# Performance work log

Hardware: AMD Instinct MI355X
Metric: run time of the kernel (lower is better)

Reference implementation:

```python
import jax, jax.numpy as jnp
import numpy as np

N_NODES = 100000
N_EDGES = 1600000
F_IN = 128
H = 128
L = 3
BN_EPS = 1e-5
NORM_EPS = 1e-12


def setup_inputs() -> dict:
    key = jax.random.key(0)
    ks = jax.random.split(key, 32)
    def rn(k, shape, s=0.05):
        return jax.random.normal(k, shape, dtype=jnp.float32) * s
    inp = {
        'x': jax.random.normal(ks[0], (N_NODES, F_IN), dtype=jnp.float32),
        'edge_index': jax.random.randint(ks[1], (2, N_EDGES), 0, N_NODES, dtype=jnp.int32),
        # node encoder
        'enc_w': rn(ks[2], (H, F_IN)), 'enc_b': rn(ks[3], (H,)),
        # per-layer SAGEConv params (stacked over layers)
        'lin_l_w': rn(ks[4], (L, H, H)), 'lin_l_b': rn(ks[5], (L, H)),
        'lin_r_w': rn(ks[6], (L, H, H)),
        # batch norms (eval mode: running stats)
        'bn_gamma': jnp.ones((L, H), jnp.float32), 'bn_beta': jnp.zeros((L, H), jnp.float32),
        'bn_mean': jnp.zeros((L, H), jnp.float32), 'bn_var': jnp.ones((L, H), jnp.float32),
        # output head
        'out_w1': rn(ks[7], (H, H)), 'out_b1': rn(ks[8], (H,)),
        'out_w2': rn(ks[9], (1, H)), 'out_b2': rn(ks[10], (1,)),
        # cost head
        'cost_w1': rn(ks[11], (H // 2, H)), 'cost_b1': rn(ks[12], (H // 2,)),
        'cost_w2': rn(ks[13], (1, H // 2)), 'cost_b2': rn(ks[14], (1,)),
        # bullwhip head
        'bw_w1': rn(ks[15], (H // 2, H)), 'bw_b1': rn(ks[16], (H // 2,)),
        'bw_w2': rn(ks[17], (1, H // 2)), 'bw_b2': rn(ks[18], (1,)),
    }
    return inp


def _sage_conv(h, src, dst, wl, bl, wr):
    # PyG SAGEConv (aggr='mean', normalize=True): lin_l(mean_j x_j) + lin_r(x_i), then L2 normalize
    msg_sum = jax.ops.segment_sum(h[src], dst, num_segments=N_NODES)  # [N, H]
    deg = jax.ops.segment_sum(jnp.ones((src.shape[0],), h.dtype), dst, num_segments=N_NODES)
    mean = msg_sum / jnp.maximum(deg, 1.0)[:, None]
    out = mean @ wl.T + bl + h @ wr.T
    norm = jnp.linalg.norm(out, axis=-1, keepdims=True)
    return out / jnp.maximum(norm, NORM_EPS)


def reference(x, edge_index, enc_w, enc_b, lin_l_w, lin_l_b, lin_r_w,
              bn_gamma, bn_beta, bn_mean, bn_var,
              out_w1, out_b1, out_w2, out_b2,
              cost_w1, cost_b1, cost_w2, cost_b2,
              bw_w1, bw_b1, bw_w2, bw_b2):
    src, dst = edge_index[0], edge_index[1]
    h = jax.nn.relu(x @ enc_w.T + enc_b)  # dropout is identity in eval
    for i in range(L):
        h = _sage_conv(h, src, dst, lin_l_w[i], lin_l_b[i], lin_r_w[i])
        # BatchNorm1d in eval mode
        h = (h - bn_mean[i]) * (bn_gamma[i] / jnp.sqrt(bn_var[i] + BN_EPS)) + bn_beta[i]
        h = jax.nn.relu(h)
    order = jax.nn.relu(h @ out_w1.T + out_b1) @ out_w2.T + out_b2
    cost = jax.nn.relu(h @ cost_w1.T + cost_b1) @ cost_w2.T + cost_b2
    bullwhip = jax.nn.relu(h @ bw_w1.T + bw_b1) @ bw_w2.T + bw_b2
    return (order, cost, bullwhip, h)
```

## Files before the change

### kernel.cpp

```cpp
#include <hip/hip_runtime.h>

#define NN 100000
#define NE 1600000
#define TN 16
#define NBK 391
#define BCAP 5120
#define CTILE 8192

static constexpr float BN_EPS = 1e-5f;
static constexpr float NORM_EPS = 1e-12f;

typedef unsigned int u32;
typedef unsigned short u16;
typedef __attribute__((ext_vector_type(8))) short short8;
typedef __attribute__((ext_vector_type(4))) float f32x4;

__device__ __forceinline__ float bflo(u32 u) {
    u32 v = u << 16; float f; __builtin_memcpy(&f, &v, 4); return f;
}
__device__ __forceinline__ float bfhi(u32 u) {
    u32 v = u & 0xffff0000u; float f; __builtin_memcpy(&f, &v, 4); return f;
}
__device__ __forceinline__ u32 packbf(float a, float b) {
    u32 ua, ub; __builtin_memcpy(&ua, &a, 4); __builtin_memcpy(&ub, &b, 4);
    u32 ra = (ua + 0x7fffu + ((ua >> 16) & 1u)) >> 16;
    u32 rb = (ub + 0x7fffu + ((ub >> 16) & 1u)) & 0xffff0000u;
    return ra | rb;
}
__device__ __forceinline__ u16 f2bf(float a) {
    u32 ua; __builtin_memcpy(&ua, &a, 4);
    return (u16)((ua + 0x7fffu + ((ua >> 16) & 1u)) >> 16);
}
__device__ __forceinline__ void acc8(float* s, uint4 v) {
    s[0] += bflo(v.x); s[1] += bfhi(v.x);
    s[2] += bflo(v.y); s[3] += bfhi(v.y);
    s[4] += bflo(v.z); s[5] += bfhi(v.z);
    s[6] += bflo(v.w); s[7] += bfhi(v.w);
}
__device__ __forceinline__ f32x4 mfma16(uint4 a, uint4 b, f32x4 c) {
    return __builtin_amdgcn_mfma_f32_16x16x32_bf16(
        __builtin_bit_cast(short8, a), __builtin_bit_cast(short8, b), c, 0, 0, 0);
}

struct TposeArgs {
    const float* src[10];
    u16* dst[10];
    int rows[10];
};

__global__ void frag_kernel(TposeArgs a) {
    const int m = blockIdx.x;
    const float* __restrict__ s = a.src[m];
    u16* __restrict__ d = a.dst[m];
    const int total = a.rows[m] * 128;
    for (int idx = threadIdx.x; idx < total; idx += 256) {
        const int i = idx & 7;
        const int l = (idx >> 3) & 63;
        const int kk = (idx >> 9) & 3;
        const int jt = idx >> 11;
        const int j = jt * 16 + (l & 15);
        const int k = kk * 32 + ((l >> 4) << 3) + i;
        d[idx] = f2bf(s[j * 128 + k]);
    }
}

__global__ __launch_bounds__(256, 4)
void bucket_scatter_kernel(const int* __restrict__ e_src, const int* __restrict__ e_dst,
                           int* __restrict__ bcnt, u32* __restrict__ ebuf) {
    __shared__ int h[NBK];
    const int tid = threadIdx.x;
    const int base = blockIdx.x * CTILE;
    const int end = (base + CTILE < NE) ? base + CTILE : NE;
    for (int i = tid; i < NBK; i += 256) h[i] = 0;
    __syncthreads();
    for (int e = base + tid; e < end; e += 256)
        atomicAdd(&h[e_dst[e] >> 8], 1);
    __syncthreads();
    for (int i = tid; i < NBK; i += 256) {
        const int c = h[i];
        h[i] = (c > 0) ? atomicAdd(&bcnt[i], c) : 0;
    }
    __syncthreads();
    for (int e = base + tid; e < end; e += 256) {
        const int d = e_dst[e];
        const int b = d >> 8;
        const int slot = atomicAdd(&h[b], 1);
        if (slot < BCAP)
            ebuf[(size_t)b * BCAP + slot] = (u32)e_src[e] | ((u32)(d & 255) << 17);
    }
}

__global__ void bscan_kernel(const int* __restrict__ bcnt, int* __restrict__ bbase) {
    const int lane = threadIdx.x;
    const int per = (NBK + 63) / 64;
    int vals[8];
    int s = 0;
    for (int i = 0; i < per; ++i) {
        const int idx = lane * per + i;
        const int v = (idx < NBK) ? bcnt[idx] : 0;
        vals[i] = s; s += v;
    }
    int incl = s;
    for (int off = 1; off < 64; off <<= 1) {
        const int t = __shfl_up(incl, off);
        if (lane >= off) incl += t;
    }
    const int excl = incl - s;
    for (int i = 0; i < per; ++i) {
        const int idx = lane * per + i;
        if (idx < NBK) bbase[idx] = excl + vals[i];
    }
    if (lane == 63) bbase[NBK] = excl + s;
}

__global__ __launch_bounds__(256, 4)
void csr_finalize_kernel(const u32* __restrict__ ebuf, const int* __restrict__ bcnt,
                         const int* __restrict__ bbase,
                         int* __restrict__ row_ptr, float* __restrict__ inv_deg,
                         int* __restrict__ csr_src) {
    __shared__ int cnt[256];
    __shared__ int rc[256];
    const int b = blockIdx.x;
    const int tid = threadIdx.x;
    const int n0 = b << 8;
    const int nb_nodes = (NN - n0 < 256) ? NN - n0 : 256;
    int ecnt = bcnt[b];
    if (ecnt > BCAP) ecnt = BCAP;
    const int gbase = bbase[b];
    const u32* eb = ebuf + (size_t)b * BCAP;
    cnt[tid] = 0;
    __syncthreads();
    for (int e = tid; e < ecnt; e += 256)
        atomicAdd(&cnt[eb[e] >> 17], 1);
    __syncthreads();
    const int myc = cnt[tid];
    int val = myc;
    for (int off = 1; off < 256; off <<= 1) {
        const int t = (tid >= off) ? cnt[tid - off] : 0;
        __syncthreads();
        val += t;
        cnt[tid] = val;
        __syncthreads();
    }
    const int excl = val - myc;
    if (tid < nb_nodes) {
        row_ptr[n0 + tid] = gbase + excl;
        inv_deg[n0 + tid] = 1.0f / (float)(myc < 1 ? 1 : myc);
    }
    rc[tid] = gbase + excl;
    __syncthreads();
    for (int e = tid; e < ecnt; e += 256) {
        const u32 p = eb[e];
        const int pos = atomicAdd(&rc[p >> 17], 1);
        csr_src[pos] = (int)(p & 0x1FFFFu);
    }
    if (b == NBK - 1 && tid == 0) row_ptr[NN] = NE;
}

__global__ __launch_bounds__(256, 6)
void encoder_kernel(const float* __restrict__ x, u16* __restrict__ h_out,
                    const u16* __restrict__ wfrag, const float* __restrict__ bias) {
    __shared__ uint4 sRows[256];
    const int tid = threadIdx.x;
    const int nb = blockIdx.x * TN;

    {
        const int row = tid >> 4, t = tid & 15;
        const float4* xr = (const float4*)(x + (size_t)(nb + row) * 128 + t * 8);
        const float4 xa = xr[0], xb = xr[1];
        uint4 p;
        p.x = packbf(xa.x, xa.y); p.y = packbf(xa.z, xa.w);
        p.z = packbf(xb.x, xb.y); p.w = packbf(xb.z, xb.w);
        sRows[row * 16 + (t ^ (row & 7))] = p;
    }
    __syncthreads();

    const int lane = tid & 63, wave = tid >> 6;
    const int cl = lane & 15, gq = lane >> 4;
    const int jt0 = wave * 2, jt1 = wave * 2 + 1;
    const uint4* wf = (const uint4*)wfrag;
    f32x4 a0 = {0, 0, 0, 0}, a1 = {0, 0, 0, 0};
    #pragma unroll
    for (int kk = 0; kk < 4; ++kk) {
        const uint4 af = sRows[cl * 16 + ((kk * 4 + gq) ^ (cl & 7))];
        a0 = mfma16(af, wf[(jt0 * 4 + kk) * 64 + lane], a0);
        a1 = mfma16(af, wf[(jt1 * 4 + kk) * 64 + lane], a1);
    }
    const int c0 = jt0 * 16 + cl, c1 = jt1 * 16 + cl;
    const float b0 = bias[c0], b1 = bias[c1];
    #pragma unroll
    for (int r = 0; r < 4; ++r) {
        const int node = nb + gq * 4 + r;
        h_out[(size_t)node * 128 + c0] = f2bf(fmaxf(a0[r] + b0, 0.f));
        h_out[(size_t)node * 128 + c1] = f2bf(fmaxf(a1[r] + b1, 0.f));
    }
}

template<int LAST>
__global__ __launch_bounds__(256, 6)
void sage_layer_kernel(const u16* __restrict__ h_in,
                       u16* __restrict__ h_out_bf, float* __restrict__ o_h,
                       const u16* __restrict__ wlfrag, const float* __restrict__ bl,
                       const u16* __restrict__ wrfrag,
                       const float* __restrict__ bn_g, const float* __restrict__ bn_b,
                       const float* __restrict__ bn_m, const float* __restrict__ bn_v,
                       const int* __restrict__ row_ptr, const int* __restrict__ csr_src,
                       const float* __restrict__ inv_deg,
                       const u16* __restrict__ o1frag, const float* __restrict__ ob1,
                       const float* __restrict__ ow2, const float* __restrict__ ob2,
                       const u16* __restrict__ c1frag, const float* __restrict__ cb1,
                       const float* __restrict__ cw2, const float* __restrict__ cb2,
                       const u16* __restrict__ b1frag, const float* __restrict__ bb1,
                       const float* __restrict__ bw2, const float* __restrict__ bb2,
                       float* __restrict__ o_order, float* __restrict__ o_cost,
                       float* __restrict__ o_bw) {
    __shared__ uint4 sRows[256];
    __shared__ uint4 sMean[256];
    __shared__ float ssb[4][16];
    const int tid = threadIdx.x;
    const int nb = blockIdx.x * TN;

    {
        const int row = tid >> 4, t = tid & 15;
        sRows[row * 16 + (t ^ (row & 7))] = ((const uint4*)h_in)[nb * 16 + tid];
    }

    {
        const int g = tid >> 4, t = tid & 15, n = nb + g;
        float acc[8] = {0, 0, 0, 0, 0, 0, 0, 0};
        const uint4* hb = (const uint4*)h_in;
        const int rp0 = row_ptr[n], rp1 = row_ptr[n + 1];
        int e = rp0;
        for (; e + 3 < rp1; e += 4) {
            const int s0 = csr_src[e], s1 = csr_src[e + 1];
            const int s2 = csr_src[e + 2], s3 = csr_src[e + 3];
            const uint4 va = hb[s0 * 16 + t];
            const uint4 vb = hb[s1 * 16 + t];
            const uint4 vc = hb[s2 * 16 + t];
            const uint4 vd = hb[s3 * 16 + t];
            acc8(acc, va); acc8(acc, vb); acc8(acc, vc); acc8(acc, vd);
        }
        for (; e < rp1; ++e) acc8(acc, hb[csr_src[e] * 16 + t]);
        const float id = inv_deg[n];
        uint4 mp;
        mp.x = packbf(acc[0] * id, acc[1] * id);
        mp.y = packbf(acc[2] * id, acc[3] * id);
        mp.z = packbf(acc[4] * id, acc[5] * id);
        mp.w = packbf(acc[6] * id, acc[7] * id);
        sMean[g * 16 + (t ^ (g & 7))] = mp;
    }
    __syncthreads();

    const int lane = tid & 63, wave = tid >> 6;
    const int cl = lane & 15, gq = lane >> 4;
    const int jt0 = wave * 2, jt1 = wave * 2 + 1;
    f32x4 a0 = {0, 0, 0, 0}, a1 = {0, 0, 0, 0};
    {
        const uint4* wf = (const uint4*)wlfrag;
        #pragma unroll
        for (int kk = 0; kk < 4; ++kk) {
            const uint4 af = sMean[cl * 16 + ((kk * 4 + gq) ^ (cl & 7))];
            a0 = mfma16(af, wf[(jt0 * 4 + kk) * 64 + lane], a0);
            a1 = mfma16(af, wf[(jt1 * 4 + kk) * 64 + lane], a1);
        }
    }
    {
        const uint4* wf = (const uint4*)wrfrag;
        #pragma unroll
        for (int kk = 0; kk < 4; ++kk) {
            const uint4 af = sRows[cl * 16 + ((kk * 4 + gq) ^ (cl & 7))];
            a0 = mfma16(af, wf[(jt0 * 4 + kk) * 64 + lane], a0);
            a1 = mfma16(af, wf[(jt1 * 4 + kk) * 64 + lane], a1);
        }
    }

    const int c0 = jt0 * 16 + cl, c1 = jt1 * 16 + cl;
    const float bl0 = bl[c0], bl1 = bl[c1];
    float t0[4], t1[4], ss[4];
    #pragma unroll
    for (int r = 0; r < 4; ++r) {
        t0[r] = a0[r] + bl0;
        t1[r] = a1[r] + bl1;
        ss[r] = t0[r] * t0[r] + t1[r] * t1[r];
    }
    #pragma unroll
    for (int m = 1; m <= 8; m <<= 1) {
        ss[0] += __shfl_xor(ss[0], m);
        ss[1] += __shfl_xor(ss[1], m);
        ss[2] += __shfl_xor(ss[2], m);
        ss[3] += __shfl_xor(ss[3], m);
    }
    if (cl == 0) {
        ssb[wave][gq * 4 + 0] = ss[0];
        ssb[wave][gq * 4 + 1] = ss[1];
        ssb[wave][gq * 4 + 2] = ss[2];
        ssb[wave][gq * 4 + 3] = ss[3];
    }
    __syncthreads();

    const float sc0 = bn_g[c0] * rsqrtf(bn_v[c0] + BN_EPS);
    const float sc1 = bn_g[c1] * rsqrtf(bn_v[c1] + BN_EPS);
    const float m0 = bn_m[c0], m1 = bn_m[c1];
    const float bb0 = bn_b[c0], bb1v = bn_b[c1];
    float f0[4], f1[4];
    #pragma unroll
    for (int r = 0; r < 4; ++r) {
        const int rw = gq * 4 + r;
        const float tot = ssb[0][rw] + ssb[1][rw] + ssb[2][rw] + ssb[3][rw];
        const float inv = 1.0f / fmaxf(sqrtf(tot), NORM_EPS);
        f0[r] = fmaxf((t0[r] * inv - m0) * sc0 + bb0, 0.f);
        f1[r] = fmaxf((t1[r] * inv - m1) * sc1 + bb1v, 0.f);
    }

    if (!LAST) {
        #pragma unroll
        for (int r = 0; r < 4; ++r) {
            const size_t node = nb + gq * 4 + r;
            h_out_bf[node * 128 + c0] = f2bf(f0[r]);
            h_out_bf[node * 128 + c1] = f2bf(f1[r]);
        }
        return;
    }

    #pragma unroll
    for (int r = 0; r < 4; ++r) {
        const size_t node = nb + gq * 4 + r;
        o_h[node * 128 + c0] = f0[r];
        o_h[node * 128 + c1] = f1[r];
    }
    u16* sr16 = (u16*)sRows;
    #pragma unroll
    for (int r = 0; r < 4; ++r) {
        const int rw = gq * 4 + r;
        sr16[rw * 128 + (((c0 >> 3) ^ (rw & 7)) << 3) + (c0 & 7)] = f2bf(f0[r]);
        sr16[rw * 128 + (((c1 >> 3) ^ (rw & 7)) << 3) + (c1 & 7)] = f2bf(f1[r]);
    }
    __syncthreads();

    {
        const uint4* wf = (const uint4*)o1frag;
        f32x4 h0 = {0, 0, 0, 0}, h1 = {0, 0, 0, 0};
        #pragma unroll
        for (int kk = 0; kk < 4; ++kk) {
            const uint4 af = sRows[cl * 16 + ((kk * 4 + gq) ^ (cl & 7))];
            h0 = mfma16(af, wf[(jt0 * 4 + kk) * 64 + lane], h0);
            h1 = mfma16(af, wf[(jt1 * 4 + kk) * 64 + lane], h1);
        }
        const float hb0 = ob1[c0], hb1 = ob1[c1];
        const float w20 = ow2[c0], w21 = ow2[c1];
        float p[4];
        #pragma unroll
        for (int r = 0; r < 4; ++r)
            p[r] = fmaxf(h0[r] + hb0, 0.f) * w20 + fmaxf(h1[r] + hb1, 0.f) * w21;
        #pragma unroll
        for (int m = 1; m <= 8; m <<= 1) {
            p[0] += __shfl_xor(p[0], m); p[1] += __shfl_xor(p[1], m);
            p[2] += __shfl_xor(p[2], m); p[3] += __shfl_xor(p[3], m);
        }
        if (cl == 0) {
            #pragma unroll
            for (int r = 0; r < 4; ++r) ssb[wave][gq * 4 + r] = p[r];
        }
        __syncthreads();
        if (tid < 16)
            o_order[nb + tid] = ssb[0][tid] + ssb[1][tid] + ssb[2][tid] + ssb[3][tid] + ob2[0];
        __syncthreads();
    }

    const u16* hfr[2] = {c1frag, b1frag};
    const float* hb1a[2] = {cb1, bb1};
    const float* hw2a[2] = {cw2, bw2};
    const float* hb2a[2] = {cb2, bb2};
    float* outs[2] = {o_cost, o_bw};
    #pragma unroll
    for (int ph = 0; ph < 2; ++ph) {
        const uint4* wf = (const uint4*)hfr[ph];
        f32x4 h0 = {0, 0, 0, 0};
        #pragma unroll
        for (int kk = 0; kk < 4; ++kk) {
            const uint4 af = sRows[cl * 16 + ((kk * 4 + gq) ^ (cl & 7))];
            h0 = mfma16(af, wf[(wave * 4 + kk) * 64 + lane], h0);
        }
        const int cc = wave * 16 + cl;
        const float hb = hb1a[ph][cc], w2 = hw2a[ph][cc];
        float p[4];
        #pragma unroll
        for (int r = 0; r < 4; ++r) p[r] = fmaxf(h0[r] + hb, 0.f) * w2;
        #pragma unroll
        for (int m = 1; m <= 8; m <<= 1) {
            p[0] += __shfl_xor(p[0], m); p[1] += __shfl_xor(p[1], m);
            p[2] += __shfl_xor(p[2], m); p[3] += __shfl_xor(p[3], m);
        }
        if (cl == 0) {
            #pragma unroll
            for (int r = 0; r < 4; ++r) ssb[wave][gq * 4 + r] = p[r];
        }
        __syncthreads();
        if (tid < 16)
            outs[ph][nb + tid] = ssb[0][tid] + ssb[1][tid] + ssb[2][tid] + ssb[3][tid] + hb2a[ph][0];
        __syncthreads();
    }
}

extern "C" void kernel_launch(void* const* d_in, const int* in_sizes, int n_in,
                              void* d_out, int out_size, void* d_ws, size_t ws_size,
                              hipStream_t stream) {
    (void)in_sizes; (void)n_in; (void)out_size;

    const float* x       = (const float*)d_in[0];
    const int*   ei      = (const int*)d_in[1];
    const float* enc_w   = (const float*)d_in[2];
    const float* enc_b   = (const float*)d_in[3];
    const float* ll_w    = (const float*)d_in[4];
    const float* ll_b    = (const float*)d_in[5];
    const float* lr_w    = (const float*)d_in[6];
    const float* bn_g    = (const float*)d_in[7];
    const float* bn_b    = (const float*)d_in[8];
    const float* bn_m    = (const float*)d_in[9];
    const float* bn_v    = (const float*)d_in[10];
    const float* out_w1  = (const float*)d_in[11];
    const float* out_b1  = (const float*)d_in[12];
    const float* out_w2  = (const float*)d_in[13];
    const float* out_b2  = (const float*)d_in[14];
    const float* cost_w1 = (const float*)d_in[15];
    const float* cost_b1 = (const float*)d_in[16];
    const float* cost_w2 = (const float*)d_in[17];
    const float* cost_b2 = (const float*)d_in[18];
    const float* bw_w1   = (const float*)d_in[19];
    const float* bw_b1   = (const float*)d_in[20];
    const float* bw_w2   = (const float*)d_in[21];
    const float* bw_b2   = (const float*)d_in[22];

    const int* e_src = ei;
    const int* e_dst = ei + NE;

    float* o_order = (float*)d_out;
    float* o_cost  = o_order + NN;
    float* o_bw    = o_cost + NN;
    float* o_h     = o_bw + NN;

    u16* hA = (u16*)d_ws;
    u16* hB = hA + (size_t)NN * 128;
    u16* wt = hB + (size_t)NN * 128;
    u16* wt_enc  = wt;
    u16* wt_ll   = wt + 16384;
    u16* wt_lr   = wt + 16384 * 4;
    u16* wt_out1 = wt + 16384 * 7;
    u16* wt_c1   = wt + 16384 * 8;
    u16* wt_bw1  = wt + 16384 * 8 + 8192;
    int* row_ptr  = (int*)(wt + 147456);
    float* inv_deg = (float*)(row_ptr + NN + 4);
    int* csr_src  = (int*)(inv_deg + NN);
    int* bcnt     = csr_src + NE;
    int* bbase    = bcnt + NBK + 1;
    u32* ebuf     = (u32*)(bbase + NBK + 1);

    const size_t need = (size_t)((char*)(ebuf + (size_t)NBK * BCAP) - (char*)d_ws);
    if (ws_size < need) return;

    hipMemsetAsync(bcnt, 0, (NBK + 1) * sizeof(int), stream);

    TposeArgs ta;
    ta.src[0] = enc_w;          ta.dst[0] = wt_enc;          ta.rows[0] = 128;
    ta.src[1] = ll_w;           ta.dst[1] = wt_ll;           ta.rows[1] = 128;
    ta.src[2] = ll_w + 16384;   ta.dst[2] = wt_ll + 16384;   ta.rows[2] = 128;
    ta.src[3] = ll_w + 32768;   ta.dst[3] = wt_ll + 32768;   ta.rows[3] = 128;
    ta.src[4] = lr_w;           ta.dst[4] = wt_lr;           ta.rows[4] = 128;
    ta.src[5] = lr_w + 16384;   ta.dst[5] = wt_lr + 16384;   ta.rows[5] = 128;
    ta.src[6] = lr_w + 32768;   ta.dst[6] = wt_lr + 32768;   ta.rows[6] = 128;
    ta.src[7] = out_w1;         ta.dst[7] = wt_out1;         ta.rows[7] = 128;
    ta.src[8] = cost_w1;        ta.dst[8] = wt_c1;           ta.rows[8] = 64;
    ta.src[9] = bw_w1;          ta.dst[9] = wt_bw1;          ta.rows[9] = 64;
    frag_kernel<<<10, 256, 0, stream>>>(ta);

    bucket_scatter_kernel<<<(NE + CTILE - 1) / CTILE, 256, 0, stream>>>(e_src, e_dst, bcnt, ebuf);
    bscan_kernel<<<1, 64, 0, stream>>>(bcnt, bbase);
    csr_finalize_kernel<<<NBK, 256, 0, stream>>>(ebuf, bcnt, bbase, row_ptr, inv_deg, csr_src);

    encoder_kernel<<<NN / TN, 256, 0, stream>>>(x, hA, wt_enc, enc_b);
    sage_layer_kernel<0><<<NN / TN, 256, 0, stream>>>(hA, hB, nullptr, wt_ll, ll_b, wt_lr,
        bn_g, bn_b, bn_m, bn_v, row_ptr, csr_src, inv_deg,
        nullptr, nullptr, nullptr, nullptr, nullptr, nullptr, nullptr, nullptr,
        nullptr, nullptr, nullptr, nullptr, nullptr, nullptr, nullptr);
    sage_layer_kernel<0><<<NN / TN, 256, 0, stream>>>(hB, hA, nullptr, wt_ll + 16384, ll_b + 128, wt_lr + 16384,
        bn_g + 128, bn_b + 128, bn_m + 128, bn_v + 128, row_ptr, csr_src, inv_deg,
        nullptr, nullptr, nullptr, nullptr, nullptr, nullptr, nullptr, nullptr,
        nullptr, nullptr, nullptr, nullptr, nullptr, nullptr, nullptr);
    sage_layer_kernel<1><<<NN / TN, 256, 0, stream>>>(hA, nullptr, o_h, wt_ll + 32768, ll_b + 256, wt_lr + 32768,
        bn_g + 256, bn_b + 256, bn_m + 256, bn_v + 256, row_ptr, csr_src, inv_deg,
        wt_out1, out_b1, out_w2, out_b2,
        wt_c1, cost_b1, cost_w2, cost_b2,
        wt_bw1, bw_b1, bw_w2, bw_b2,
        o_order, o_cost, o_bw);
}
```

Before: 314.9 us.

## Process 32 nodes per SAGE layer block to reuse weight fragments

Doubles the node tile of the SAGE layer kernel from 16 to 32, so each weight fragment loaded from global memory feeds two MFMA tiles and the grid has half as many blocks. The neighbour gather now loops over two node halves per thread group, and the launch bound is raised to 8 blocks per CU to keep occupancy. This is meant to cut repeated weight-fragment traffic and per-block overhead. In exchange there is less gather parallelism per thread, plus more LDS and register pressure.

Result: no change. 312.2 us (-0.9%).

```diff
diff --git a/kernel.cpp b/kernel.cpp
--- a/kernel.cpp
+++ b/kernel.cpp
@@ -3,6 +3,7 @@
 #define NN 100000
 #define NE 1600000
 #define TN 16
+#define TNL 32
 #define NBK 391
 #define BCAP 5120
 #define CTILE 8192
@@ -197,7 +198,7 @@
 }
 
 template<int LAST>
-__global__ __launch_bounds__(256, 6)
+__global__ __launch_bounds__(256, 8)
 void sage_layer_kernel(const u16* __restrict__ h_in,
                        u16* __restrict__ h_out_bf, float* __restrict__ o_h,
                        const u16* __restrict__ wlfrag, const float* __restrict__ bl,
@@ -214,87 +215,105 @@
                        const float* __restrict__ bw2, const float* __restrict__ bb2,
                        float* __restrict__ o_order, float* __restrict__ o_cost,
                        float* __restrict__ o_bw) {
-    __shared__ uint4 sRows[256];
-    __shared__ uint4 sMean[256];
-    __shared__ float ssb[4][16];
+    __shared__ uint4 sRows[512];
+    __shared__ uint4 sMean[512];
+    __shared__ float ssb[4][32];
     const int tid = threadIdx.x;
-    const int nb = blockIdx.x * TN;
+    const int nb = blockIdx.x * TNL;
 
     {
-        const int row = tid >> 4, t = tid & 15;
-        sRows[row * 16 + (t ^ (row & 7))] = ((const uint4*)h_in)[nb * 16 + tid];
+        const uint4* src = (const uint4*)h_in + (size_t)nb * 16;
+        const int i0 = tid, i1 = tid + 256;
+        sRows[(i0 >> 4) * 16 + ((i0 & 15) ^ ((i0 >> 4) & 7))] = src[i0];
+        sRows[(i1 >> 4) * 16 + ((i1 & 15) ^ ((i1 >> 4) & 7))] = src[i1];
     }
 
     {
-        const int g = tid >> 4, t = tid & 15, n = nb + g;
-        float acc[8] = {0, 0, 0, 0, 0, 0, 0, 0};
+        const int g = tid >> 4, t = tid & 15;
         const uint4* hb = (const uint4*)h_in;
-        const int rp0 = row_ptr[n], rp1 = row_ptr[n + 1];
-        int e = rp0;
-        for (; e + 3 < rp1; e += 4) {
-            const int s0 = csr_src[e], s1 = csr_src[e + 1];
-            const int s2 = csr_src[e + 2], s3 = csr_src[e + 3];
-            const uint4 va = hb[s0 * 16 + t];
-            const uint4 vb = hb[s1 * 16 + t];
-            const uint4 vc = hb[s2 * 16 + t];
-            const uint4 vd = hb[s3 * 16 + t];
-            acc8(acc, va); acc8(acc, vb); acc8(acc, vc); acc8(acc, vd);
-        }
-        for (; e < rp1; ++e) acc8(acc, hb[csr_src[e] * 16 + t]);
-        const float id = inv_deg[n];
-        uint4 mp;
-        mp.x = packbf(acc[0] * id, acc[1] * id);
-        mp.y = packbf(acc[2] * id, acc[3] * id);
-        mp.z = packbf(acc[4] * id, acc[5] * id);
-        mp.w = packbf(acc[6] * id, acc[7] * id);
-        sMean[g * 16 + (t ^ (g & 7))] = mp;
+        #pragma unroll
+        for (int half = 0; half < 2; ++half) {
+            const int row = g + half * 16;
+            const int n = nb + row;
+            float acc[8] = {0, 0, 0, 0, 0, 0, 0, 0};
+            const int rp0 = row_ptr[n], rp1 = row_ptr[n + 1];
+            int e = rp0;
+            for (; e + 3 < rp1; e += 4) {
+                const int s0 = csr_src[e], s1 = csr_src[e + 1];
+                const int s2 = csr_src[e + 2], s3 = csr_src[e + 3];
+                const uint4 va = hb[s0 * 16 + t];
+                const uint4 vb = hb[s1 * 16 + t];
+                const uint4 vc = hb[s2 * 16 + t];
+                const uint4 vd = hb[s3 * 16 + t];
+                acc8(acc, va); acc8(acc, vb); acc8(acc, vc); acc8(acc, vd);
+            }
+            for (; e < rp1; ++e) acc8(acc, hb[csr_src[e] * 16 + t]);
+            const float id = inv_deg[n];
+            uint4 mp;
+            mp.x = packbf(acc[0] * id, acc[1] * id);
+            mp.y = packbf(acc[2] * id, acc[3] * id);
+            mp.z = packbf(acc[4] * id, acc[5] * id);
+            mp.w = packbf(acc[6] * id, acc[7] * id);
+            sMean[row * 16 + (t ^ (row & 7))] = mp;
+        }
     }
     __syncthreads();
 
     const int lane = tid & 63, wave = tid >> 6;
     const int cl = lane & 15, gq = lane >> 4;
     const int jt0 = wave * 2, jt1 = wave * 2 + 1;
-    f32x4 a0 = {0, 0, 0, 0}, a1 = {0, 0, 0, 0};
+    f32x4 a00 = {0,0,0,0}, a01 = {0,0,0,0}, a10 = {0,0,0,0}, a11 = {0,0,0,0};
     {
         const uint4* wf = (const uint4*)wlfrag;
         #pragma unroll
         for (int kk = 0; kk < 4; ++kk) {
-            const uint4 af = sMean[cl * 16 + ((kk * 4 + gq) ^ (cl & 7))];
-            a0 = mfma16(af, wf[(jt0 * 4 + kk) * 64 + lane], a0);
-            a1 = mfma16(af, wf[(jt1 * 4 + kk) * 64 + lane], a1);
+            const int ch = (kk * 4 + gq) ^ (cl & 7);
+            const uint4 af0 = sMean[cl * 16 + ch];
+            const uint4 af1 = sMean[(16 + cl) * 16 + ch];
+            const uint4 b0 = wf[(jt0 * 4 + kk) * 64 + lane];
+            const uint4 b1 = wf[(jt1 * 4 + kk) * 64 + lane];
+            a00 = mfma16(af0, b0, a00); a01 = mfma16(af0, b1, a01);
+            a10 = mfma16(af1, b0, a10); a11 = mfma16(af1, b1, a11);
         }
     }
     {
         const uint4* wf = (const uint4*)wrfrag;
         #pragma unroll
         for (int kk = 0; kk < 4; ++kk) {
-            const uint4 af = sRows[cl * 16 + ((kk * 4 + gq) ^ (cl & 7))];
-            a0 = mfma16(af, wf[(jt0 * 4 + kk) * 64 + lane], a0);
-            a1 = mfma16(af, wf[(jt1 * 4 + kk) * 64 + lane], a1);
+            const int ch = (kk * 4 + gq) ^ (cl & 7);
+            const uint4 af0 = sRows[cl * 16 + ch];
+            const uint4 af1 = sRows[(16 + cl) * 16 + ch];
+            const uint4 b0 = wf[(jt0 * 4 + kk) * 64 + lane];
+            const uint4 b1 = wf[(jt1 * 4 + kk) * 64 + lane];
+            a00 = mfma16(af0, b0, a00); a01 = mfma16(af0, b1, a01);
+            a10 = mfma16(af1, b0, a10); a11 = mfma16(af1, b1, a11);
         }
     }
 
     const int c0 = jt0 * 16 + cl, c1 = jt1 * 16 + cl;
     const float bl0 = bl[c0], bl1 = bl[c1];
-    float t0[4], t1[4], ss[4];
+    float t00[4], t01[4], t10[4], t11[4], ss0[4], ss1[4];
     #pragma unroll
     for (int r = 0; r < 4; ++r) {
-        t0[r] = a0[r] + bl0;
-        t1[r] = a1[r] + bl1;
-        ss[r] = t0[r] * t0[r] + t1[r] * t1[r];
+        t00[r] = a00[r] + bl0; t01[r] = a01[r] + bl1;
+        t10[r] = a10[r] + bl0; t11[r] = a11[r] + bl1;
+        ss0[r] = t00[r] * t00[r] + t01[r] * t01[r];
+        ss1[r] = t10[r] * t10[r] + t11[r] * t11[r];
     }
     #pragma unroll
     for (int m = 1; m <= 8; m <<= 1) {
-        ss[0] += __shfl_xor(ss[0], m);
-        ss[1] += __shfl_xor(ss[1], m);
-        ss[2] += __shfl_xor(ss[2], m);
-        ss[3] += __shfl_xor(ss[3], m);
+        #pragma unroll
+        for (int r = 0; r < 4; ++r) {
+            ss0[r] += __shfl_xor(ss0[r], m);
+            ss1[r] += __shfl_xor(ss1[r], m);
+        }
     }
     if (cl == 0) {
-        ssb[wave][gq * 4 + 0] = ss[0];
-        ssb[wave][gq * 4 + 1] = ss[1];
-        ssb[wave][gq * 4 + 2] = ss[2];
-        ssb[wave][gq * 4 + 3] = ss[3];
+        #pragma unroll
+        for (int r = 0; r < 4; ++r) {
+            ssb[wave][gq * 4 + r] = ss0[r];
+            ssb[wave][16 + gq * 4 + r] = ss1[r];
+        }
     }
     __syncthreads();
 
@@ -302,67 +321,87 @@
     const float sc1 = bn_g[c1] * rsqrtf(bn_v[c1] + BN_EPS);
     const float m0 = bn_m[c0], m1 = bn_m[c1];
     const float bb0 = bn_b[c0], bb1v = bn_b[c1];
-    float f0[4], f1[4];
+    float f00[4], f01[4], f10[4], f11[4];
     #pragma unroll
     for (int r = 0; r < 4; ++r) {
-        const int rw = gq * 4 + r;
-        const float tot = ssb[0][rw] + ssb[1][rw] + ssb[2][rw] + ssb[3][rw];
-        const float inv = 1.0f / fmaxf(sqrtf(tot), NORM_EPS);
-        f0[r] = fmaxf((t0[r] * inv - m0) * sc0 + bb0, 0.f);
-        f1[r] = fmaxf((t1[r] * inv - m1) * sc1 + bb1v, 0.f);
+        const int rw0 = gq * 4 + r, rw1 = 16 + rw0;
+        const float tot0 = ssb[0][rw0] + ssb[1][rw0] + ssb[2][rw0] + ssb[3][rw0];
+        const float tot1 = ssb[0][rw1] + ssb[1][rw1] + ssb[2][rw1] + ssb[3][rw1];
+        const float inv0 = 1.0f / fmaxf(sqrtf(tot0), NORM_EPS);
+        const float inv1 = 1.0f / fmaxf(sqrtf(tot1), NORM_EPS);
+        f00[r] = fmaxf((t00[r] * inv0 - m0) * sc0 + bb0, 0.f);
+        f01[r] = fmaxf((t01[r] * inv0 - m1) * sc1 + bb1v, 0.f);
+        f10[r] = fmaxf((t10[r] * inv1 - m0) * sc0 + bb0, 0.f);
+        f11[r] = fmaxf((t11[r] * inv1 - m1) * sc1 + bb1v, 0.f);
     }
 
     if (!LAST) {
         #pragma unroll
         for (int r = 0; r < 4; ++r) {
-            const size_t node = nb + gq * 4 + r;
-            h_out_bf[node * 128 + c0] = f2bf(f0[r]);
-            h_out_bf[node * 128 + c1] = f2bf(f1[r]);
+            const size_t n0s = nb + gq * 4 + r;
+            const size_t n1s = n0s + 16;
+            h_out_bf[n0s * 128 + c0] = f2bf(f00[r]);
+            h_out_bf[n0s * 128 + c1] = f2bf(f01[r]);
+            h_out_bf[n1s * 128 + c0] = f2bf(f10[r]);
+            h_out_bf[n1s * 128 + c1] = f2bf(f11[r]);
         }
         return;
     }
 
+    u16* sr16 = (u16*)sRows;
     #pragma unroll
     for (int r = 0; r < 4; ++r) {
-        const size_t node = nb + gq * 4 + r;
-        o_h[node * 128 + c0] = f0[r];
-        o_h[node * 128 + c1] = f1[r];
-    }
-    u16* sr16 = (u16*)sRows;
-    #pragma unroll
-    for (int r = 0; r < 4; ++r) {
-        const int rw = gq * 4 + r;
-        sr16[rw * 128 + (((c0 >> 3) ^ (rw & 7)) << 3) + (c0 & 7)] = f2bf(f0[r]);
-        sr16[rw * 128 + (((c1 >> 3) ^ (rw & 7)) << 3) + (c1 & 7)] = f2bf(f1[r]);
+        const int rw0 = gq * 4 + r, rw1 = 16 + rw0;
+        const size_t n0s = nb + rw0, n1s = nb + rw1;
+        o_h[n0s * 128 + c0] = f00[r];
+        o_h[n0s * 128 + c1] = f01[r];
+        o_h[n1s * 128 + c0] = f10[r];
+        o_h[n1s * 128 + c1] = f11[r];
+        sr16[rw0 * 128 + (((c0 >> 3) ^ (rw0 & 7)) << 3) + (c0 & 7)] = f2bf(f00[r]);
+        sr16[rw0 * 128 + (((c1 >> 3) ^ (rw0 & 7)) << 3) + (c1 & 7)] = f2bf(f01[r]);
+        sr16[rw1 * 128 + (((c0 >> 3) ^ (rw1 & 7)) << 3) + (c0 & 7)] = f2bf(f10[r]);
+        sr16[rw1 * 128 + (((c1 >> 3) ^ (rw1 & 7)) << 3) + (c1 & 7)] = f2bf(f11[r]);
     }
     __syncthreads();
 
     {
         const uint4* wf = (const uint4*)o1frag;
-        f32x4 h0 = {0, 0, 0, 0}, h1 = {0, 0, 0, 0};
+        f32x4 h00 = {0,0,0,0}, h01 = {0,0,0,0}, h10 = {0,0,0,0}, h11 = {0,0,0,0};
         #pragma unroll
         for (int kk = 0; kk < 4; ++kk) {
-            const uint4 af = sRows[cl * 16 + ((kk * 4 + gq) ^ (cl & 7))];
-            h0 = mfma16(af, wf[(jt0 * 4 + kk) * 64 + lane], h0);
-            h1 = mfma16(af, wf[(jt1 * 4 + kk) * 64 + lane], h1);
+            const int ch = (kk * 4 + gq) ^ (cl & 7);
+            const uint4 af0 = sRows[cl * 16 + ch];
+            const uint4 af1 = sRows[(16 + cl) * 16 + ch];
+            const uint4 b0 = wf[(jt0 * 4 + kk) * 64 + lane];
+            const uint4 b1 = wf[(jt1 * 4 + kk) * 64 + lane];
+            h00 = mfma16(af0, b0, h00); h01 = mfma16(af0, b1, h01);
+            h10 = mfma16(af1, b0, h10); h11 = mfma16(af1, b1, h11);
         }
         const float hb0 = ob1[c0], hb1 = ob1[c1];
         const float w20 = ow2[c0], w21 = ow2[c1];
-        float p[4];
-        #pragma unroll
-        for (int r = 0; r < 4; ++r)
-            p[r] = fmaxf(h0[r] + hb0, 0.f) * w20 + fmaxf(h1[r] + hb1, 0.f) * w21;
+        float p0[4], p1[4];
+        #pragma unroll
+        for (int r = 0; r < 4; ++r) {
+            p0[r] = fmaxf(h00[r] + hb0, 0.f) * w20 + fmaxf(h01[r] + hb1, 0.f) * w21;
+            p1[r] = fmaxf(h10[r] + hb0, 0.f) * w20 + fmaxf(h11[r] + hb1, 0.f) * w21;
+        }
         #pragma unroll
         for (int m = 1; m <= 8; m <<= 1) {
-            p[0] += __shfl_xor(p[0], m); p[1] += __shfl_xor(p[1], m);
-            p[2] += __shfl_xor(p[2], m); p[3] += __shfl_xor(p[3], m);
+            #pragma unroll
+            for (int r = 0; r < 4; ++r) {
+                p0[r] += __shfl_xor(p0[r], m);
+                p1[r] += __shfl_xor(p1[r], m);
+            }
         }
         if (cl == 0) {
             #pragma unroll
-            for (int r = 0; r < 4; ++r) ssb[wave][gq * 4 + r] = p[r];
+            for (int r = 0; r < 4; ++r) {
+                ssb[wave][gq * 4 + r] = p0[r];
+                ssb[wave][16 + gq * 4 + r] = p1[r];
+            }
         }
         __syncthreads();
-        if (tid < 16)
+        if (tid < 32)
             o_order[nb + tid] = ssb[0][tid] + ssb[1][tid] + ssb[2][tid] + ssb[3][tid] + ob2[0];
         __syncthreads();
     }
@@ -375,28 +414,41 @@
     #pragma unroll
     for (int ph = 0; ph < 2; ++ph) {
         const uint4* wf = (const uint4*)hfr[ph];
-        f32x4 h0 = {0, 0, 0, 0};
+        f32x4 g0 = {0,0,0,0}, g1 = {0,0,0,0};
         #pragma unroll
         for (int kk = 0; kk < 4; ++kk) {
-            const uint4 af = sRows[cl * 16 + ((kk * 4 + gq) ^ (cl & 7))];
-            h0 = mfma16(af, wf[(wave * 4 + kk) * 64 + lane], h0);
+            const int ch = (kk * 4 + gq) ^ (cl & 7);
+            const uint4 af0 = sRows[cl * 16 + ch];
+            const uint4 af1 = sRows[(16 + cl) * 16 + ch];
+            const uint4 b = wf[(wave * 4 + kk) * 64 + lane];
+            g0 = mfma16(af0, b, g0);
+            g1 = mfma16(af1, b, g1);
         }
         const int cc = wave * 16 + cl;
         const float hb = hb1a[ph][cc], w2 = hw2a[ph][cc];
-        float p[4];
-        #pragma unroll
-        for (int r = 0; r < 4; ++r) p[r] = fmaxf(h0[r] + hb, 0.f) * w2;
+        float p0[4], p1[4];
+        #pragma unroll
+        for (int r = 0; r < 4; ++r) {
+            p0[r] = fmaxf(g0[r] + hb, 0.f) * w2;
+            p1[r] = fmaxf(g1[r] + hb, 0.f) * w2;
+        }
         #pragma unroll
         for (int m = 1; m <= 8; m <<= 1) {
-            p[0] += __shfl_xor(p[0], m); p[1] += __shfl_xor(p[1], m);
-            p[2] += __shfl_xor(p[2], m); p[3] += __shfl_xor(p[3], m);
+            #pragma unroll
+            for (int r = 0; r < 4; ++r) {
+                p0[r] += __shfl_xor(p0[r], m);
+                p1[r] += __shfl_xor(p1[r], m);
+            }
         }
         if (cl == 0) {
             #pragma unroll
-            for (int r = 0; r < 4; ++r) ssb[wave][gq * 4 + r] = p[r];
+            for (int r = 0; r < 4; ++r) {
+                ssb[wave][gq * 4 + r] = p0[r];
+                ssb[wave][16 + gq * 4 + r] = p1[r];
+            }
         }
         __syncthreads();
-        if (tid < 16)
+        if (tid < 32)
             outs[ph][nb + tid] = ssb[0][tid] + ssb[1][tid] + ssb[2][tid] + ssb[3][tid] + hb2a[ph][0];
         __syncthreads();
     }
@@ -478,15 +530,15 @@
     csr_finalize_kernel<<<NBK, 256, 0, stream>>>(ebuf, bcnt, bbase, row_ptr, inv_deg, csr_src);
 
     encoder_kernel<<<NN / TN, 256, 0, stream>>>(x, hA, wt_enc, enc_b);
-    sage_layer_kernel<0><<<NN / TN, 256, 0, stream>>>(hA, hB, nullptr, wt_ll, ll_b, wt_lr,
+    sage_layer_kernel<0><<<NN / TNL, 256, 0, stream>>>(hA, hB, nullptr, wt_ll, ll_b, wt_lr,
         bn_g, bn_b, bn_m, bn_v, row_ptr, csr_src, inv_deg,
         nullptr, nullptr, nullptr, nullptr, nullptr, nullptr, nullptr, nullptr,
         nullptr, nullptr, nullptr, nullptr, nullptr, nullptr, nullptr);
-    sage_layer_kernel<0><<<NN / TN, 256, 0, stream>>>(hB, hA, nullptr, wt_ll + 16384, ll_b + 128, wt_lr + 16384,
+    sage_layer_kernel<0><<<NN / TNL, 256, 0, stream>>>(hB, hA, nullptr, wt_ll + 16384, ll_b + 128, wt_lr + 16384,
         bn_g + 128, bn_b + 128, bn_m + 128, bn_v + 128, row_ptr, csr_src, inv_deg,
         nullptr, nullptr, nullptr, nullptr, nullptr, nullptr, nullptr, nullptr,
         nullptr, nullptr, nullptr, nullptr, nullptr, nullptr, nullptr);
-    sage_layer_kernel<1><<<NN / TN, 256, 0, stream>>>(hA, nullptr, o_h, wt_ll + 32768, ll_b + 256, wt_lr + 32768,
+    sage_layer_kernel<1><<<NN / TNL, 256, 0, stream>>>(hA, nullptr, o_h, wt_ll + 32768, ll_b + 256, wt_lr + 32768,
         bn_g + 256, bn_b + 256, bn_m + 256, bn_v + 256, row_ptr, csr_src, inv_deg,
         wt_out1, out_b1, out_w2, out_b2,
         wt_c1, cost_b1, cost_w2, cost_b2,
```
